# Performance work log

Hardware: AMD Instinct MI355X
Metric: run time of the kernel (lower is better)

Reference implementation:

```python
import jax, jax.numpy as jnp
import numpy as np

N_NODES = 50000
N_EDGES = 800000
NFEAT, NHID, NHEAD, NCLASS = 512, 64, 8, 40
NEG_SLOPE = 0.2  # LeakyReLU alpha from __init__


def setup_inputs() -> dict:
    key = jax.random.key(0)
    ks = jax.random.split(key, 8)
    glorot = lambda k, shape: jax.random.normal(k, shape, jnp.float32) * (2.0 / (shape[-2] + shape[-1])) ** 0.5
    return {
        "x": jax.random.normal(ks[0], (N_NODES, NFEAT), jnp.float32),
        "edge_list": jax.random.randint(ks[1], (2, N_EDGES), 0, N_NODES, jnp.int32),
        # nhead input-layer GATconv params: weight [H, nfeat, nhid], att [H, 2*nhid], bias [H, nhid]
        "W1": glorot(ks[2], (NHEAD, NFEAT, NHID)),
        "a1": jax.random.normal(ks[3], (NHEAD, 2 * NHID), jnp.float32) * 0.1,
        "b1": jnp.zeros((NHEAD, NHID), jnp.float32),
        # single output-head GATconv: [nhid*nhead, nclass]
        "W2": glorot(ks[4], (NHEAD * NHID, NCLASS)),
        "a2": jax.random.normal(ks[5], (2 * NCLASS,), jnp.float32) * 0.1,
        "b2": jnp.zeros((NCLASS,), jnp.float32),
    }


def _gat_layer(x, W, a, b, src, dst, n_nodes):
    """One GATconv head (eval mode, dropout = identity)."""
    h = x @ W                                  # [N, F]
    f = W.shape[-1]
    s_src = h @ a[:f]                          # [N] per-node src score
    s_dst = h @ a[f:]                          # [N] per-node dst score
    e = jax.nn.leaky_relu(s_src[src] + s_dst[dst], NEG_SLOPE)  # [E]
    # segment softmax over incoming edges of each dst node (numerically stable)
    m = jax.ops.segment_max(e, dst, num_segments=n_nodes)
    m = jax.lax.stop_gradient(jnp.where(jnp.isfinite(m), m, 0.0))
    w = jnp.exp(e - m[dst])
    denom = jax.ops.segment_sum(w, dst, num_segments=n_nodes)
    alpha = w / jnp.maximum(denom[dst], 1e-16)                 # [E]
    out = jax.ops.segment_sum(alpha[:, None] * h[src], dst, num_segments=n_nodes)
    return out + b


def reference(x, edge_list, W1, a1, b1, W2, a2, b2):
    n = x.shape[0]
    src, dst = edge_list[0], edge_list[1]
    # multi-head input layer, concat along feature dim
    heads = jax.vmap(lambda W, a, b: _gat_layer(x, W, a, b, src, dst, n))(W1, a1, b1)  # [H, N, nhid]
    h = jax.nn.elu(jnp.transpose(heads, (1, 0, 2)).reshape(n, -1))                      # [N, H*nhid]
    # single output head (mean over nhead_out=1)
    out = _gat_layer(h, W2, a2, b2, src, dst, n)                                        # [N, nclass]
    return jax.nn.log_softmax(out, axis=1)
```

## Files before the change

kernel.cpp:

```cpp
#include <hip/hip_runtime.h>
#include <math.h>

#define N_NODES 50000
#define N_EDGES 800000
#define NFEAT 512
#define NHID 64
#define NHEAD 8
#define NCLASS 40
#define NEG_SLOPE 0.2f

#define N_RT 3125
#define N_RT_PAD 3128
#define SCAN_NBLK 49
#define CASTX_NBLK 12512
#define PACK_NBLK (CASTX_NBLK + 140)

typedef __attribute__((ext_vector_type(8))) short short8;
typedef __attribute__((ext_vector_type(4))) short short4v;
typedef __attribute__((ext_vector_type(4))) float f32x4;

__device__ __forceinline__ float bf2f(short s) {
    return __uint_as_float(((unsigned)(unsigned short)s) << 16);
}
__device__ __forceinline__ short f2bf(float f) {
    unsigned u = __float_as_uint(f);
    unsigned r = (u + 0x7FFFu + ((u >> 16) & 1u)) >> 16;
    return (short)(unsigned short)r;
}



__global__ void count_deg(const int* __restrict__ el, int* __restrict__ deg) {
    int e = blockIdx.x * blockDim.x + threadIdx.x;
    if (e < N_EDGES) atomicAdd(&deg[el[N_EDGES + e]], 1);
}

__global__ __launch_bounds__(256) void scan1(const int* __restrict__ deg,
                                             int* __restrict__ loc,
                                             int* __restrict__ bsum) {
    int tid = threadIdx.x, lane = tid & 63, w = tid >> 6;
    int base = blockIdx.x * 1024 + tid * 4;
    int d0 = (base + 0 < N_NODES) ? deg[base + 0] : 0;
    int d1 = (base + 1 < N_NODES) ? deg[base + 1] : 0;
    int d2 = (base + 2 < N_NODES) ? deg[base + 2] : 0;
    int d3 = (base + 3 < N_NODES) ? deg[base + 3] : 0;
    int s0 = d0, s1 = s0 + d1, s2 = s1 + d2, s3 = s2 + d3;
    int t = s3;
#pragma unroll
    for (int d = 1; d < 64; d <<= 1) {
        int u = __shfl_up(t, d);
        if (lane >= d) t += u;
    }
    __shared__ int wsum[4];
    if (lane == 63) wsum[w] = t;
    __syncthreads();
    int woff = 0;
#pragma unroll
    for (int j = 0; j < 4; ++j) woff += (j < w) ? wsum[j] : 0;
    int excl = woff + t - s3;
    if (base + 0 < N_NODES) loc[base + 0] = excl + s0;
    if (base + 1 < N_NODES) loc[base + 1] = excl + s1;
    if (base + 2 < N_NODES) loc[base + 2] = excl + s2;
    if (base + 3 < N_NODES) loc[base + 3] = excl + s3;
    if (tid == 255) bsum[blockIdx.x] = woff + t;
}

__global__ void scan2(const int* __restrict__ bsum, int* __restrict__ boff) {
    int lane = threadIdx.x;
    int v = (lane < SCAN_NBLK) ? bsum[lane] : 0;
    int t = v;
#pragma unroll
    for (int d = 1; d < 64; d <<= 1) {
        int u = __shfl_up(t, d);
        if (lane >= d) t += u;
    }
    if (lane < SCAN_NBLK) boff[lane] = t - v;
}

__global__ __launch_bounds__(256) void scan3(const int* __restrict__ deg,
                                             const int* __restrict__ loc,
                                             const int* __restrict__ boff,
                                             int* __restrict__ ptr,
                                             int* __restrict__ cursor) {
    int base = blockIdx.x * 1024 + threadIdx.x * 4;
    int off = boff[blockIdx.x];
    if (blockIdx.x == 0 && threadIdx.x == 0) ptr[0] = 0;
#pragma unroll
    for (int k = 0; k < 4; ++k) {
        int i = base + k;
        if (i < N_NODES) {
            int P = off + loc[i];
            ptr[i + 1] = P;
            cursor[i] = P - deg[i];
        }
    }
}

__global__ void scatter_k(const int* __restrict__ el, int* __restrict__ cursor,
                          int* __restrict__ esrc) {
    int e = blockIdx.x * blockDim.x + threadIdx.x;
    if (e >= N_EDGES) return;
    int dst = el[N_EDGES + e];
    int p = atomicAdd(&cursor[dst], 1);
    esrc[p] = el[e];
}

__global__ __launch_bounds__(256) void pack_k(const float* __restrict__ x,
                                              const float* __restrict__ W1,
                                              const float* __restrict__ W2,
                                              short* __restrict__ xp,
                                              short* __restrict__ Wp1,
                                              short* __restrict__ Wp2) {
    if (blockIdx.x < CASTX_NBLK) {
        int t = blockIdx.x * 256 + threadIdx.x;
        int l = t & 63, ks = (t >> 6) & 15, rt = t >> 10;
        short8 o;
        if (rt >= N_RT) {
#pragma unroll
            for (int j = 0; j < 8; ++j) o[j] = 0;
        } else {
            int row = rt * 16 + (l & 15);
            int col = ks * 32 + (l >> 4) * 8;
            const float* p = x + (size_t)row * NFEAT + col;
            float4 v0 = *(const float4*)p;
            float4 v1 = *(const float4*)(p + 4);
            o[0] = f2bf(v0.x); o[1] = f2bf(v0.y); o[2] = f2bf(v0.z); o[3] = f2bf(v0.w);
            o[4] = f2bf(v1.x); o[5] = f2bf(v1.y); o[6] = f2bf(v1.z); o[7] = f2bf(v1.w);
        }
        *(short8*)(xp + (size_t)t * 8) = o;
        return;
    }
    int t = (blockIdx.x - CASTX_NBLK) * 256 + threadIdx.x;
    if (t < 32768) {
        int l = t & 63, ct = (t >> 6) & 7, ks = (t >> 9) & 15, g = t >> 13;
        int c = g * 128 + ct * 16 + (l & 15);
        int head = c >> 6, f = c & 63;
        int k0 = ks * 32 + (l >> 4) * 8;
        short8 o;
#pragma unroll
        for (int j = 0; j < 8; ++j)
            o[j] = f2bf(W1[(size_t)head * NFEAT * NHID + (k0 + j) * NHID + f]);
        *(short8*)(Wp1 + (size_t)t * 8) = o;
    } else if (t < 32768 + 3072) {
        int u = t - 32768;
        int l = u & 63;
        int kc = u >> 6;
        int ct2 = kc % 3, ks = kc / 3;
        int col = ct2 * 16 + (l & 15);
        short8 o;
#pragma unroll
        for (int j = 0; j < 8; ++j) {
            int kp = ks * 32 + (l >> 4) * 8 + j;
            int head = kp >> 6, fp = kp & 63;
            int l15 = fp >> 2, ctp = fp & 3;
            int ct = ((head & 1) << 2) | ctp;
            int gg = head >> 1;
            int orig_k = gg * 128 + ct * 16 + l15;
            o[j] = (col < NCLASS) ? f2bf(W2[(size_t)orig_k * NCLASS + col]) : (short)0;
        }
        *(short8*)(Wp2 + (size_t)u * 8) = o;
    }
}

__global__ __launch_bounds__(256, 2) void gemm1(const short* __restrict__ xp,
                                                const short* __restrict__ Wp1,
                                                const float* __restrict__ a1,
                                                short* __restrict__ h1p,
                                                float* __restrict__ s1s,
                                                float* __restrict__ s1d) {
    int w = threadIdx.x >> 6, l = threadIdx.x & 63;
    int g = w;
    int rt0 = blockIdx.x * 2;
    f32x4 acc[2][8];
#pragma unroll
    for (int i = 0; i < 2; ++i)
#pragma unroll
        for (int ct = 0; ct < 8; ++ct) acc[i][ct] = (f32x4){0.f, 0.f, 0.f, 0.f};

    const short* aP0 = xp + ((size_t)rt0 * 16 * 64 + l) * 8;
    const short* aP1 = xp + ((size_t)(rt0 + 1) * 16 * 64 + l) * 8;
    const short* bP  = Wp1 + (size_t)g * 16 * 4096 + l * 8;

    short8 a0c = *(const short8*)aP0;
    short8 a1c = *(const short8*)aP1;
    short8 bc[8];
#pragma unroll
    for (int ct = 0; ct < 8; ++ct) bc[ct] = *(const short8*)(bP + ct * 512);

    for (int ks = 0; ks < 16; ++ks) {
        int kn = (ks < 15) ? ks + 1 : ks;
        short8 a0n = *(const short8*)(aP0 + kn * 512);
        short8 a1n = *(const short8*)(aP1 + kn * 512);
        short8 bn[8];
#pragma unroll
        for (int ct = 0; ct < 8; ++ct) bn[ct] = *(const short8*)(bP + kn * 4096 + ct * 512);
#pragma unroll
        for (int ct = 0; ct < 8; ++ct) {
            acc[0][ct] = __builtin_amdgcn_mfma_f32_16x16x32_bf16(a0c, bc[ct], acc[0][ct], 0, 0, 0);
            acc[1][ct] = __builtin_amdgcn_mfma_f32_16x16x32_bf16(a1c, bc[ct], acc[1][ct], 0, 0, 0);
        }
        a0c = a0n; a1c = a1n;
#pragma unroll
        for (int ct = 0; ct < 8; ++ct) bc[ct] = bn[ct];
    }

    float avs[8], avd[8];
#pragma unroll
    for (int ct = 0; ct < 8; ++ct) {
        int head = 2 * g + (ct >> 2);
        int f = (ct & 3) * 16 + (l & 15);
        avs[ct] = a1[head * 128 + f];
        avd[ct] = a1[head * 128 + 64 + f];
    }
    int l15 = l & 15;
    int rbase = (l >> 4) * 4;
#pragma unroll
    for (int i = 0; i < 2; ++i)
#pragma unroll
        for (int r = 0; r < 4; ++r) {
            int row = (rt0 + i) * 16 + rbase + r;
            float ps0 = 0.f, pd0 = 0.f, ps1 = 0.f, pd1 = 0.f;
#pragma unroll
            for (int ct = 0; ct < 4; ++ct) {
                ps0 += acc[i][ct][r] * avs[ct];
                pd0 += acc[i][ct][r] * avd[ct];
            }
#pragma unroll
            for (int ct = 4; ct < 8; ++ct) {
                ps1 += acc[i][ct][r] * avs[ct];
                pd1 += acc[i][ct][r] * avd[ct];
            }
#pragma unroll
            for (int mask = 1; mask < 16; mask <<= 1) {
                ps0 += __shfl_xor(ps0, mask);
                pd0 += __shfl_xor(pd0, mask);
                ps1 += __shfl_xor(ps1, mask);
                pd1 += __shfl_xor(pd1, mask);
            }
            if (row < N_NODES) {
                if (l15 == 0) {
                    s1s[row * 8 + 2 * g]     = ps0;
                    s1d[row * 8 + 2 * g]     = pd0;
                    s1s[row * 8 + 2 * g + 1] = ps1;
                    s1d[row * 8 + 2 * g + 1] = pd1;
                }
                short4v o0, o1;
#pragma unroll
                for (int c = 0; c < 4; ++c) { o0[c] = f2bf(acc[i][c][r]); o1[c] = f2bf(acc[i][4 + c][r]); }
                size_t base = (size_t)row * 512 + g * 128 + l15 * 4;
                *(short4v*)(h1p + base) = o0;
                *(short4v*)(h1p + base + 64) = o1;
            }
        }
}

__global__ __launch_bounds__(256) void att1(const int* __restrict__ ptr,
                                            const int* __restrict__ esrc,
                                            const float* __restrict__ s1s,
                                            const float* __restrict__ s1d,
                                            const short* __restrict__ h1p,
                                            const float* __restrict__ b1,
                                            short* __restrict__ hcatp) {
    int n = blockIdx.x * 4 + (threadIdx.x >> 6);
    int l = threadIdx.x & 63;
    if (n >= N_NODES) return;
    int beg = ptr[n], end = ptr[n + 1];
    int h = l >> 3;
    float sd = s1d[n * 8 + h];
    float den = 0.f;
    float acc[8] = {0.f, 0.f, 0.f, 0.f, 0.f, 0.f, 0.f, 0.f};
    if (beg < end) {
        int src = esrc[beg];
        short8 hv = *(const short8*)(h1p + (size_t)src * 512 + l * 8);
        float ss = s1s[src * 8 + h];
        for (int i = beg; i < end; ++i) {
            int ip = (i + 1 < end) ? i + 1 : i;
            int nsrc = esrc[ip];
            short8 nhv = *(const short8*)(h1p + (size_t)nsrc * 512 + l * 8);
            float nss = s1s[nsrc * 8 + h];
            float sc = ss + sd;
            sc = fmaxf(sc, NEG_SLOPE * sc);
            float wgt = __expf(sc);
            den += wgt;
#pragma unroll
            for (int j = 0; j < 8; ++j) acc[j] += wgt * bf2f(hv[j]);
            hv = nhv; ss = nss;
        }
    }
    float rden = 1.f / fmaxf(den, 1e-16f);
    short8 o;
#pragma unroll
    for (int j = 0; j < 8; ++j) {
        int forig = (j & 3) * 16 + (l & 7) * 2 + (j >> 2);
        float v = acc[j] * rden + b1[h * 64 + forig];
        v = v > 0.f ? v : (__expf(v) - 1.f);
        o[j] = f2bf(v);
    }
    size_t addr = (((size_t)(n >> 4) * 16 + (l >> 2)) * 64 + (l & 3) * 16 + (n & 15)) * 8;
    *(short8*)(hcatp + addr) = o;
}

__global__ __launch_bounds__(256) void gemm2(const short* __restrict__ hcatp,
                                             const short* __restrict__ Wp2,
                                             const float* __restrict__ a2,
                                             short* __restrict__ h2,
                                             float* __restrict__ s2s,
                                             float* __restrict__ s2d) {
    int w = threadIdx.x >> 6, l = threadIdx.x & 63;
    int rt = blockIdx.x * 4 + w;
    f32x4 acc[3];
#pragma unroll
    for (int ct = 0; ct < 3; ++ct) acc[ct] = (f32x4){0.f, 0.f, 0.f, 0.f};
#pragma unroll 2
    for (int ks = 0; ks < 16; ++ks) {
        short8 a = *(const short8*)(hcatp + ((size_t)(rt * 16 + ks) * 64 + l) * 8);
        const short* bp = Wp2 + (size_t)(ks * 3) * 512 + l * 8;
#pragma unroll
        for (int ct = 0; ct < 3; ++ct) {
            short8 b = *(const short8*)(bp + ct * 512);
            acc[ct] = __builtin_amdgcn_mfma_f32_16x16x32_bf16(a, b, acc[ct], 0, 0, 0);
        }
    }
    float ps[4] = {0.f, 0.f, 0.f, 0.f}, pd[4] = {0.f, 0.f, 0.f, 0.f};
    int cl = l & 15, rb = (l >> 4) * 4;
#pragma unroll
    for (int ct = 0; ct < 3; ++ct) {
        int col = ct * 16 + cl;
        if (col < NCLASS) {
#pragma unroll
            for (int r = 0; r < 4; ++r) {
                ps[r] += acc[ct][r] * a2[col];
                pd[r] += acc[ct][r] * a2[NCLASS + col];
                int row = rt * 16 + rb + r;
                if (row < N_NODES) h2[(size_t)row * NCLASS + col] = f2bf(acc[ct][r]);
            }
        }
    }
#pragma unroll
    for (int mask = 1; mask < 16; mask <<= 1)
#pragma unroll
        for (int r = 0; r < 4; ++r) {
            ps[r] += __shfl_xor(ps[r], mask);
            pd[r] += __shfl_xor(pd[r], mask);
        }
    if (cl == 0) {
#pragma unroll
        for (int r = 0; r < 4; ++r) {
            int row = rt * 16 + rb + r;
            if (row < N_NODES) { s2s[row] = ps[r]; s2d[row] = pd[r]; }
        }
    }
}

__global__ __launch_bounds__(256) void att2(const int* __restrict__ ptr,
                                            const int* __restrict__ esrc,
                                            const float* __restrict__ s2s,
                                            const float* __restrict__ s2d,
                                            const short* __restrict__ h2,
                                            const float* __restrict__ b2,
                                            float* __restrict__ out) {
    int n = blockIdx.x * 4 + (threadIdx.x >> 6);
    int l = threadIdx.x & 63;
    if (n >= N_NODES) return;
    int beg = ptr[n], end = ptr[n + 1];
    float sd = s2d[n];
    float den = 0.f, acc = 0.f;
    if (beg < end) {
        int src = esrc[beg];
        float hv = (l < NCLASS) ? bf2f(h2[(size_t)src * NCLASS + l]) : 0.f;
        float ss = s2s[src];
        for (int i = beg; i < end; ++i) {
            int ip = (i + 1 < end) ? i + 1 : i;
            int nsrc = esrc[ip];
            float nhv = (l < NCLASS) ? bf2f(h2[(size_t)nsrc * NCLASS + l]) : 0.f;
            float nss = s2s[nsrc];
            float sc = ss + sd;
            sc = fmaxf(sc, NEG_SLOPE * sc);
            float wgt = __expf(sc);
            den += wgt;
            acc += wgt * hv;
            hv = nhv; ss = nss;
        }
    }
    float v = (l < NCLASS) ? acc / fmaxf(den, 1e-16f) + b2[l] : -INFINITY;
    float mx = v;
#pragma unroll
    for (int o = 32; o; o >>= 1) mx = fmaxf(mx, __shfl_down(mx, o));
    mx = __shfl(mx, 0);
    float ex = (l < NCLASS) ? __expf(v - mx) : 0.f;
    float s = ex;
#pragma unroll
    for (int o = 32; o; o >>= 1) s += __shfl_down(s, o);
    s = __shfl(s, 0);
    float ls = __logf(s);
    if (l < NCLASS) out[(size_t)n * NCLASS + l] = v - mx - ls;
}


extern "C" void kernel_launch(void* const* d_in, const int* in_sizes, int n_in,
                              void* d_out, int out_size, void* d_ws, size_t ws_size,
                              hipStream_t stream) {
    const float* x  = (const float*)d_in[0];
    const int*   el = (const int*)d_in[1];
    const float* W1 = (const float*)d_in[2];
    const float* a1 = (const float*)d_in[3];
    const float* b1 = (const float*)d_in[4];
    const float* W2 = (const float*)d_in[5];
    const float* a2 = (const float*)d_in[6];
    const float* b2 = (const float*)d_in[7];
    float* out = (float*)d_out;

    short* sbase = (short*)d_ws;
    short* xp    = sbase;
    short* hcatp = sbase + 25624576;
    short* h1p   = sbase + 51249152;
    short* Wp1   = sbase + 76849152;
    short* Wp2   = sbase + 77111296;
    short* h2    = sbase + 77135872;
    float* fbase = (float*)(sbase + 79135872);
    float* s1s   = fbase;
    float* s1d   = fbase + 400000;
    float* s2s   = fbase + 800000;
    float* s2d   = fbase + 850000;
    int*   ibase = (int*)(fbase + 900000);
    int*   deg    = ibase;
    int*   ptr    = ibase + 50000;
    int*   cursor = ibase + 100001;
    int*   esrc   = ibase + 150001;
    int*   loc    = ibase + 950001;
    int*   bsum   = ibase + 1000001;
    int*   boff   = ibase + 1000065;

    hipMemsetAsync(deg, 0, (size_t)N_NODES * 4, stream);
    count_deg<<<(N_EDGES + 255) / 256, 256, 0, stream>>>(el, deg);
    scan1<<<SCAN_NBLK, 256, 0, stream>>>(deg, loc, bsum);
    scan2<<<1, 64, 0, stream>>>(bsum, boff);
    scan3<<<SCAN_NBLK, 256, 0, stream>>>(deg, loc, boff, ptr, cursor);
    scatter_k<<<(N_EDGES + 255) / 256, 256, 0, stream>>>(el, cursor, esrc);

    pack_k<<<PACK_NBLK, 256, 0, stream>>>(x, W1, W2, xp, Wp1, Wp2);

    gemm1<<<N_RT_PAD / 2, 256, 0, stream>>>(xp, Wp1, a1, h1p, s1s, s1d);
    att1<<<(N_NODES + 3) / 4, 256, 0, stream>>>(ptr, esrc, s1s, s1d, h1p, b1, hcatp);

    gemm2<<<N_RT_PAD / 4, 256, 0, stream>>>(hcatp, Wp2, a2, h2, s2s, s2d);
    att2<<<(N_NODES + 3) / 4, 256, 0, stream>>>(ptr, esrc, s2s, s2d, h2, b2, out);
}
```

Baseline: 550.2 us.

## Fuse x bf16 cast into gemm1 via LDS staging, drop scan2 and packed hcat layout

Removes the separate pass that cast x to a packed bf16 buffer. gemm1 now loads the fp32 rows directly, converts them and stages the A tiles in shared memory, which avoids writing and rereading roughly 50 MB of intermediate data. The scan2 kernel is folded into scan3, with each block reducing the preceding block sums itself, saving one launch. att1 now writes hcat in row-major order and gemm2 reads it with strided row loads. The cost is an LDS stage plus a barrier in gemm1, and less coalesced A loads in gemm2.

```diff
diff --git a/kernel.cpp b/kernel.cpp
--- a/kernel.cpp
+++ b/kernel.cpp
@@ -12,8 +12,6 @@
 #define N_RT 3125
 #define N_RT_PAD 3128
 #define SCAN_NBLK 49
-#define CASTX_NBLK 12512
-#define PACK_NBLK (CASTX_NBLK + 140)
 
 typedef __attribute__((ext_vector_type(8))) short short8;
 typedef __attribute__((ext_vector_type(4))) short short4v;
@@ -65,25 +63,22 @@
     if (tid == 255) bsum[blockIdx.x] = woff + t;
 }
 
-__global__ void scan2(const int* __restrict__ bsum, int* __restrict__ boff) {
-    int lane = threadIdx.x;
-    int v = (lane < SCAN_NBLK) ? bsum[lane] : 0;
-    int t = v;
-#pragma unroll
-    for (int d = 1; d < 64; d <<= 1) {
-        int u = __shfl_up(t, d);
-        if (lane >= d) t += u;
-    }
-    if (lane < SCAN_NBLK) boff[lane] = t - v;
-}
-
 __global__ __launch_bounds__(256) void scan3(const int* __restrict__ deg,
                                              const int* __restrict__ loc,
-                                             const int* __restrict__ boff,
+                                             const int* __restrict__ bsum,
                                              int* __restrict__ ptr,
                                              int* __restrict__ cursor) {
+    __shared__ int sOff;
+    if (threadIdx.x < 64) {
+        int lane = threadIdx.x;
+        int v = (lane < SCAN_NBLK && lane < (int)blockIdx.x) ? bsum[lane] : 0;
+#pragma unroll
+        for (int m = 1; m < 64; m <<= 1) v += __shfl_xor(v, m);
+        if (lane == 0) sOff = v;
+    }
+    __syncthreads();
+    int off = sOff;
     int base = blockIdx.x * 1024 + threadIdx.x * 4;
-    int off = boff[blockIdx.x];
     if (blockIdx.x == 0 && threadIdx.x == 0) ptr[0] = 0;
 #pragma unroll
     for (int k = 0; k < 4; ++k) {
@@ -105,32 +100,11 @@
     esrc[p] = el[e];
 }
 
-__global__ __launch_bounds__(256) void pack_k(const float* __restrict__ x,
-                                              const float* __restrict__ W1,
+__global__ __launch_bounds__(256) void pack_w(const float* __restrict__ W1,
                                               const float* __restrict__ W2,
-                                              short* __restrict__ xp,
                                               short* __restrict__ Wp1,
                                               short* __restrict__ Wp2) {
-    if (blockIdx.x < CASTX_NBLK) {
-        int t = blockIdx.x * 256 + threadIdx.x;
-        int l = t & 63, ks = (t >> 6) & 15, rt = t >> 10;
-        short8 o;
-        if (rt >= N_RT) {
-#pragma unroll
-            for (int j = 0; j < 8; ++j) o[j] = 0;
-        } else {
-            int row = rt * 16 + (l & 15);
-            int col = ks * 32 + (l >> 4) * 8;
-            const float* p = x + (size_t)row * NFEAT + col;
-            float4 v0 = *(const float4*)p;
-            float4 v1 = *(const float4*)(p + 4);
-            o[0] = f2bf(v0.x); o[1] = f2bf(v0.y); o[2] = f2bf(v0.z); o[3] = f2bf(v0.w);
-            o[4] = f2bf(v1.x); o[5] = f2bf(v1.y); o[6] = f2bf(v1.z); o[7] = f2bf(v1.w);
-        }
-        *(short8*)(xp + (size_t)t * 8) = o;
-        return;
-    }
-    int t = (blockIdx.x - CASTX_NBLK) * 256 + threadIdx.x;
+    int t = blockIdx.x * 256 + threadIdx.x;
     if (t < 32768) {
         int l = t & 63, ct = (t >> 6) & 7, ks = (t >> 9) & 15, g = t >> 13;
         int c = g * 128 + ct * 16 + (l & 15);
@@ -162,44 +136,63 @@
     }
 }
 
-__global__ __launch_bounds__(256, 2) void gemm1(const short* __restrict__ xp,
+__global__ __launch_bounds__(256, 2) void gemm1(const float* __restrict__ x,
                                                 const short* __restrict__ Wp1,
                                                 const float* __restrict__ a1,
                                                 short* __restrict__ h1p,
                                                 float* __restrict__ s1s,
                                                 float* __restrict__ s1d) {
+    __shared__ short As[2 * 16 * 64 * 8];
     int w = threadIdx.x >> 6, l = threadIdx.x & 63;
     int g = w;
     int rt0 = blockIdx.x * 2;
+    int row0 = rt0 * 16;
+
+#pragma unroll
+    for (int u = 0; u < 8; ++u) {
+        int idx = threadIdx.x + u * 256;
+        int rl = idx >> 6, cg = idx & 63;
+        int row = row0 + rl;
+        short8 o;
+        if (row < N_NODES) {
+            const float* p = x + (size_t)row * NFEAT + cg * 8;
+            float4 v0 = *(const float4*)p;
+            float4 v1 = *(const float4*)(p + 4);
+            o[0] = f2bf(v0.x); o[1] = f2bf(v0.y); o[2] = f2bf(v0.z); o[3] = f2bf(v0.w);
+            o[4] = f2bf(v1.x); o[5] = f2bf(v1.y); o[6] = f2bf(v1.z); o[7] = f2bf(v1.w);
+        } else {
+#pragma unroll
+            for (int j = 0; j < 8; ++j) o[j] = 0;
+        }
+        int rtl = rl >> 4, rloc = rl & 15, ks = cg >> 2, sub = cg & 3;
+        int lane = rloc + sub * 16;
+        *(short8*)(As + (((rtl * 16 + ks) * 64) + lane) * 8) = o;
+    }
+    __syncthreads();
+
     f32x4 acc[2][8];
 #pragma unroll
     for (int i = 0; i < 2; ++i)
 #pragma unroll
         for (int ct = 0; ct < 8; ++ct) acc[i][ct] = (f32x4){0.f, 0.f, 0.f, 0.f};
 
-    const short* aP0 = xp + ((size_t)rt0 * 16 * 64 + l) * 8;
-    const short* aP1 = xp + ((size_t)(rt0 + 1) * 16 * 64 + l) * 8;
-    const short* bP  = Wp1 + (size_t)g * 16 * 4096 + l * 8;
-
-    short8 a0c = *(const short8*)aP0;
-    short8 a1c = *(const short8*)aP1;
+    const short* bP = Wp1 + (size_t)g * 16 * 4096 + l * 8;
     short8 bc[8];
 #pragma unroll
     for (int ct = 0; ct < 8; ++ct) bc[ct] = *(const short8*)(bP + ct * 512);
 
     for (int ks = 0; ks < 16; ++ks) {
         int kn = (ks < 15) ? ks + 1 : ks;
-        short8 a0n = *(const short8*)(aP0 + kn * 512);
-        short8 a1n = *(const short8*)(aP1 + kn * 512);
         short8 bn[8];
 #pragma unroll
         for (int ct = 0; ct < 8; ++ct) bn[ct] = *(const short8*)(bP + kn * 4096 + ct * 512);
+        short8 a0 = *(const short8*)(As + ((ks)*64 + l) * 8);
+        short8 a1v = *(const short8*)(As + ((16 + ks) * 64 + l) * 8);
 #pragma unroll
         for (int ct = 0; ct < 8; ++ct) {
-            acc[0][ct] = __builtin_amdgcn_mfma_f32_16x16x32_bf16(a0c, bc[ct], acc[0][ct], 0, 0, 0);
-            acc[1][ct] = __builtin_amdgcn_mfma_f32_16x16x32_bf16(a1c, bc[ct], acc[1][ct], 0, 0, 0);
-        }
-        a0c = a0n; a1c = a1n;
+            acc[0][ct] = __builtin_amdgcn_mfma_f32_16x16x32_bf16(a0, bc[ct], acc[0][ct], 0, 0, 0);
+            acc[1][ct] = __builtin_amdgcn_mfma_f32_16x16x32_bf16(a1v, bc[ct], acc[1][ct], 0, 0, 0);
+        }
 #pragma unroll
         for (int ct = 0; ct < 8; ++ct) bc[ct] = bn[ct];
     }
@@ -260,7 +253,7 @@
                                             const float* __restrict__ s1d,
                                             const short* __restrict__ h1p,
                                             const float* __restrict__ b1,
-                                            short* __restrict__ hcatp) {
+                                            short* __restrict__ hcat) {
     int n = blockIdx.x * 4 + (threadIdx.x >> 6);
     int l = threadIdx.x & 63;
     if (n >= N_NODES) return;
@@ -296,11 +289,10 @@
         v = v > 0.f ? v : (__expf(v) - 1.f);
         o[j] = f2bf(v);
     }
-    size_t addr = (((size_t)(n >> 4) * 16 + (l >> 2)) * 64 + (l & 3) * 16 + (n & 15)) * 8;
-    *(short8*)(hcatp + addr) = o;
-}
-
-__global__ __launch_bounds__(256) void gemm2(const short* __restrict__ hcatp,
+    *(short8*)(hcat + (size_t)n * 512 + l * 8) = o;
+}
+
+__global__ __launch_bounds__(256) void gemm2(const short* __restrict__ hcat,
                                              const short* __restrict__ Wp2,
                                              const float* __restrict__ a2,
                                              short* __restrict__ h2,
@@ -308,12 +300,14 @@
                                              float* __restrict__ s2d) {
     int w = threadIdx.x >> 6, l = threadIdx.x & 63;
     int rt = blockIdx.x * 4 + w;
+    int arow = rt * 16 + (l & 15);
+    const short* aBase = hcat + (size_t)arow * 512 + (l >> 4) * 8;
     f32x4 acc[3];
 #pragma unroll
     for (int ct = 0; ct < 3; ++ct) acc[ct] = (f32x4){0.f, 0.f, 0.f, 0.f};
 #pragma unroll 2
     for (int ks = 0; ks < 16; ++ks) {
-        short8 a = *(const short8*)(hcatp + ((size_t)(rt * 16 + ks) * 64 + l) * 8);
+        short8 a = *(const short8*)(aBase + ks * 32);
         const short* bp = Wp2 + (size_t)(ks * 3) * 512 + l * 8;
 #pragma unroll
         for (int ct = 0; ct < 3; ++ct) {
@@ -411,8 +405,7 @@
     float* out = (float*)d_out;
 
     short* sbase = (short*)d_ws;
-    short* xp    = sbase;
-    short* hcatp = sbase + 25624576;
+    short* hcat  = sbase + 25624576;
     short* h1p   = sbase + 51249152;
     short* Wp1   = sbase + 76849152;
     short* Wp2   = sbase + 77111296;
@@ -429,20 +422,18 @@
     int*   esrc   = ibase + 150001;
     int*   loc    = ibase + 950001;
     int*   bsum   = ibase + 1000001;
-    int*   boff   = ibase + 1000065;
 
     hipMemsetAsync(deg, 0, (size_t)N_NODES * 4, stream);
     count_deg<<<(N_EDGES + 255) / 256, 256, 0, stream>>>(el, deg);
     scan1<<<SCAN_NBLK, 256, 0, stream>>>(deg, loc, bsum);
-    scan2<<<1, 64, 0, stream>>>(bsum, boff);
-    scan3<<<SCAN_NBLK, 256, 0, stream>>>(deg, loc, boff, ptr, cursor);
+    scan3<<<SCAN_NBLK, 256, 0, stream>>>(deg, loc, bsum, ptr, cursor);
     scatter_k<<<(N_EDGES + 255) / 256, 256, 0, stream>>>(el, cursor, esrc);
 
-    pack_k<<<PACK_NBLK, 256, 0, stream>>>(x, W1, W2, xp, Wp1, Wp2);
-
-    gemm1<<<N_RT_PAD / 2, 256, 0, stream>>>(xp, Wp1, a1, h1p, s1s, s1d);
-    att1<<<(N_NODES + 3) / 4, 256, 0, stream>>>(ptr, esrc, s1s, s1d, h1p, b1, hcatp);
-
-    gemm2<<<N_RT_PAD / 4, 256, 0, stream>>>(hcatp, Wp2, a2, h2, s2s, s2d);
+    pack_w<<<140, 256, 0, stream>>>(W1, W2, Wp1, Wp2);
+
+    gemm1<<<N_RT_PAD / 2, 256, 0, stream>>>(x, Wp1, a1, h1p, s1s, s1d);
+    att1<<<(N_NODES + 3) / 4, 256, 0, stream>>>(ptr, esrc, s1s, s1d, h1p, b1, hcat);
+
+    gemm2<<<N_RT_PAD / 4, 256, 0, stream>>>(hcat, Wp2, a2, h2, s2s, s2d);
     att2<<<(N_NODES + 3) / 4, 256, 0, stream>>>(ptr, esrc, s2s, s2d, h2, b2, out);
 }
```

After: 545.8 us. About the same (-0.8%).
